# Kernel tuning notes

Hardware: AMD Instinct MI355X
Metric: run time of the kernel (lower is better)

## Reference

```python
import jax, jax.numpy as jnp
import numpy as np

NUM_USERS = 100000
NUM_ITEMS = 100000
N_NODES = NUM_USERS + NUM_ITEMS
EMB = 64
N_EDGES = 3200000
N_LAYERS = 3


def setup_inputs() -> dict:
    key = jax.random.key(0)
    k1, k2, k3, k4, k5 = jax.random.split(key, 5)
    user_emb = jax.random.normal(k1, (NUM_USERS, EMB), dtype=jnp.float32)
    item_emb = jax.random.normal(k2, (NUM_ITEMS, EMB), dtype=jnp.float32)
    # COO representation of the normalized adjacency norm_adj (values ~ 1/sqrt(d_i d_j))
    edge_row = jax.random.randint(k3, (N_EDGES,), 0, N_NODES, dtype=jnp.int32)
    edge_col = jax.random.randint(k4, (N_EDGES,), 0, N_NODES, dtype=jnp.int32)
    edge_w = jax.random.uniform(k5, (N_EDGES,), dtype=jnp.float32)
    return {"user_emb": user_emb, "item_emb": item_emb, "edge_w": edge_w,
            "edge_row": edge_row, "edge_col": edge_col}


def _spmm(edge_row, edge_col, edge_w, x):
    # y[r] = sum_{e: row[e]==r} w[e] * x[col[e]]  ==  torch.sparse.mm(norm_adj, x)
    msgs = edge_w[:, None] * x[edge_col]  # [n_edges, E]
    return jax.ops.segment_sum(msgs, edge_row, num_segments=N_NODES)


def reference(user_emb, item_emb, edge_w, edge_row, edge_col):
    ego = jnp.concatenate([user_emb, item_emb], axis=0)  # [N, E]
    acc = jnp.zeros_like(ego)
    for _ in range(N_LAYERS):
        ego = _spmm(edge_row, edge_col, edge_w, ego)
        acc = acc + ego
    final = acc / N_LAYERS  # mean over the n_layers propagated embeddings
    user_all = final[:NUM_USERS]
    item_all = final[NUM_USERS:]
    return (user_all, item_all)
```

## Files before the change

kernel.cpp:

```cpp
#include <hip/hip_runtime.h>
#include <hip/hip_bf16.h>


constexpr int NUM_USERS = 100000;
constexpr int NUM_ITEMS = 100000;
constexpr int N_NODES   = NUM_USERS + NUM_ITEMS;
constexpr int EMB       = 64;
constexpr int N_EDGES   = 3200000;

constexpr int BUCK_SHIFT = 8;
constexpr int NBUCK = (N_NODES + 255) >> BUCK_SHIFT;
constexpr int BIN_BLOCK = 512;
constexpr int EPB = 8192;
constexpr int NBIN_BLOCKS = (N_EDGES + EPB - 1) / EPB;
constexpr int SORT_CAP = 6144;

constexpr int HIST_BLOCKS   = 512;
constexpr int CONCAT_BLOCKS = (N_NODES * 8 + 255) / 256;

constexpr int ROWS_PER_BLOCK = 32;
constexpr int ECAP = 1536;


__device__ __forceinline__ float bfl(unsigned u) { return __uint_as_float(u << 16); }
__device__ __forceinline__ float bfh(unsigned u) { return __uint_as_float(u & 0xFFFF0000u); }
__device__ __forceinline__ unsigned f2bf(float f) {
    unsigned u = __float_as_uint(f);
    return (u + 0x7FFFu + ((u >> 16) & 1u)) >> 16;
}
__device__ __forceinline__ unsigned pk(float lo, float hi) {
    return f2bf(lo) | (f2bf(hi) << 16);
}


__global__ __launch_bounds__(256) void prep(
    const int* __restrict__ row, int* __restrict__ bcnt,
    const float4* __restrict__ u, const float4* __restrict__ it,
    uint4* __restrict__ ebuf) {
    __shared__ int h[NBUCK];
    if (blockIdx.x < HIST_BLOCKS) {
        for (int i = threadIdx.x; i < NBUCK; i += 256) h[i] = 0;
        __syncthreads();
        int nt = HIST_BLOCKS * 256;
        for (int e = blockIdx.x * 256 + threadIdx.x; e < N_EDGES; e += nt) {
            int r = __builtin_nontemporal_load(&row[e]);
            atomicAdd(&h[r >> BUCK_SHIFT], 1);
        }
        __syncthreads();
        for (int i = threadIdx.x; i < NBUCK; i += 256) {
            int c = h[i];
            if (c) atomicAdd(&bcnt[i], c);
        }
    } else {
        int i = (blockIdx.x - HIST_BLOCKS) * 256 + threadIdx.x;
        if (i >= N_NODES * 8) return;
        const float4* s = (i < NUM_USERS * 8) ? (u + 2 * (size_t)i)
                                              : (it + 2 * ((size_t)i - (size_t)NUM_USERS * 8));
        float4 f0 = s[0], f1 = s[1];
        uint4 o;
        o.x = pk(f0.x, f0.y); o.y = pk(f0.z, f0.w);
        o.z = pk(f1.x, f1.y); o.w = pk(f1.z, f1.w);
        ebuf[i] = o;
    }
}


__global__ __launch_bounds__(1024) void scan_buckets(const int* __restrict__ bcnt,
                                                     int* __restrict__ bbase,
                                                     int* __restrict__ bcursor) {
    __shared__ int lds[1024];
    int t = threadIdx.x;
    int v = (t < NBUCK) ? bcnt[t] : 0;
    lds[t] = v;
    __syncthreads();
    for (int off = 1; off < 1024; off <<= 1) {
        int x = (t >= off) ? lds[t - off] : 0;
        __syncthreads();
        lds[t] += x;
        __syncthreads();
    }
    int excl = lds[t] - v;
    if (t < NBUCK) { bbase[t] = excl; bcursor[t] = excl; }
    if (t == 0) bbase[NBUCK] = N_EDGES;
}

__global__ __launch_bounds__(BIN_BLOCK) void bin_edges(
    const int* __restrict__ row, const int* __restrict__ col,
    const float* __restrict__ w,
    int* __restrict__ bcursor,
    unsigned* __restrict__ binned_cw, unsigned char* __restrict__ binned_rl) {
    __shared__ unsigned      stage_cw[EPB];
    __shared__ unsigned char stage_rl[EPB];
    __shared__ int  hcnt[NBUCK];
    __shared__ int  hbase[NBUCK];
    __shared__ int  cursor[NBUCK];
    __shared__ int  lds2[BIN_BLOCK];
    int t = threadIdx.x;
    int e0 = blockIdx.x * EPB;
    int e1 = e0 + EPB; if (e1 > N_EDGES) e1 = N_EDGES;

    for (int i = t; i < NBUCK; i += BIN_BLOCK) hcnt[i] = 0;
    __syncthreads();
    for (int e = e0 + t; e < e1; e += BIN_BLOCK)
        atomicAdd(&hcnt[row[e] >> BUCK_SHIFT], 1);
    __syncthreads();

    for (int i = t; i < NBUCK; i += BIN_BLOCK) {
        int c = hcnt[i];
        hbase[i] = c ? atomicAdd(&bcursor[i], c) : 0;
    }
    int i0 = 2 * t, i1 = 2 * t + 1;
    int c0 = (i0 < NBUCK) ? hcnt[i0] : 0;
    int c1 = (i1 < NBUCK) ? hcnt[i1] : 0;
    lds2[t] = c0 + c1;
    __syncthreads();
    for (int off = 1; off < BIN_BLOCK; off <<= 1) {
        int x = (t >= off) ? lds2[t - off] : 0;
        __syncthreads();
        lds2[t] += x;
        __syncthreads();
    }
    int pairExcl = lds2[t] - (c0 + c1);
    if (i0 < NBUCK) cursor[i0] = pairExcl;
    if (i1 < NBUCK) cursor[i1] = pairExcl + c0;
    __syncthreads();

    for (int e = e0 + t; e < e1; e += BIN_BLOCK) {
        int r  = row[e];
        int bk = r >> BUCK_SHIFT;
        int pos = atomicAdd(&cursor[bk], 1);
        float wv = __builtin_nontemporal_load(&w[e]);
        unsigned q = (unsigned)(wv * 16384.f + 0.5f);
        if (q > 16383u) q = 16383u;
        stage_cw[pos] = (unsigned)__builtin_nontemporal_load(&col[e]) | (q << 18);
        stage_rl[pos] = (unsigned char)(r & 255);
    }
    __syncthreads();

    int wave = t >> 6;
    int lane = t & 63;
    int sl   = lane & 7;
    constexpr int NWAVE = BIN_BLOCK / 64;
    for (int base = wave * 8; base < NBUCK; base += NWAVE * 8) {
        int bk = base + (lane >> 3);
        if (bk < NBUCK) {
            int c  = hcnt[bk];
            int st = cursor[bk] - c;
            int gp = hbase[bk];
            for (int j = sl; j < c; j += 8) {
                binned_cw[gp + j] = stage_cw[st + j];
                binned_rl[gp + j] = stage_rl[st + j];
            }
        }
    }
}

__global__ __launch_bounds__(256) void sort_bucket(
    const int* __restrict__ bbase,
    const unsigned* __restrict__ binned_cw, const unsigned char* __restrict__ binned_rl,
    unsigned* __restrict__ sorted, int* __restrict__ row_start) {
    __shared__ unsigned      raw_cw[SORT_CAP];
    __shared__ unsigned char raw_rl[SORT_CAP];
    __shared__ unsigned      buf[SORT_CAP];
    __shared__ int cnt[256];
    __shared__ int sc[256];
    int b = blockIdx.x, t = threadIdx.x;
    int gb = bbase[b];
    int n  = bbase[b + 1] - gb;
    int m  = n < SORT_CAP ? n : SORT_CAP;

    cnt[t] = 0;
    for (int i = t; i < m; i += 256) {
        raw_cw[i] = binned_cw[gb + i];
        raw_rl[i] = binned_rl[gb + i];
    }
    __syncthreads();
    for (int i = t; i < m; i += 256)
        atomicAdd(&cnt[raw_rl[i]], 1);
    __syncthreads();

    int v = cnt[t];
    sc[t] = v;
    __syncthreads();
    for (int off = 1; off < 256; off <<= 1) {
        int x = (t >= off) ? sc[t - off] : 0;
        __syncthreads();
        sc[t] += x;
        __syncthreads();
    }
    int excl = sc[t] - v;

    int r = (b << BUCK_SHIFT) + t;
    if (r < N_NODES) row_start[r] = gb + excl;
    if (b == NBUCK - 1 && t == 0) row_start[N_NODES] = N_EDGES;
    __syncthreads();
    cnt[t] = excl;
    __syncthreads();

    for (int i = t; i < m; i += 256) {
        int k = atomicAdd(&cnt[raw_rl[i]], 1);
        buf[k] = raw_cw[i];
    }
    __syncthreads();
    for (int i = t; i < m; i += 256)
        sorted[gb + i] = buf[i];
}


template<bool LAST>
__global__ __launch_bounds__(256) void spmm_bf16(
    const int* __restrict__ row_start, const unsigned* __restrict__ sorted,
    const uint4* __restrict__ src,
    uint4* __restrict__ y,
    const uint4* __restrict__ y1,
    float4* __restrict__ out)
{
    __shared__ unsigned erec[ECAP];
    __shared__ int rs[ROWS_PER_BLOCK + 1];
    int t  = threadIdx.x;
    int R0 = blockIdx.x * ROWS_PER_BLOCK;
    if (t <= ROWS_PER_BLOCK) rs[t] = row_start[R0 + t];
    __syncthreads();
    int eb0 = rs[0];
    int n   = rs[ROWS_PER_BLOCK] - eb0;

    int g = t >> 3;
    int s = t & 7;
    int r = R0 + g;
    int s0 = rs[g], s1 = rs[g + 1];
    int cnt = s1 - s0;

    float a0 = 0.f, a1 = 0.f, a2 = 0.f, a3 = 0.f;
    float a4 = 0.f, a5 = 0.f, a6 = 0.f, a7 = 0.f;
    constexpr float WSC = 1.0f / 16384.f;

#define ACC(vv, wt) \
    a0 = fmaf(wt, bfl(vv.x), a0); a1 = fmaf(wt, bfh(vv.x), a1); \
    a2 = fmaf(wt, bfl(vv.y), a2); a3 = fmaf(wt, bfh(vv.y), a3); \
    a4 = fmaf(wt, bfl(vv.z), a4); a5 = fmaf(wt, bfh(vv.z), a5); \
    a6 = fmaf(wt, bfl(vv.w), a6); a7 = fmaf(wt, bfh(vv.w), a7);

    if (n <= ECAP) {
        for (int i = t; i < n; i += 256) erec[i] = sorted[eb0 + i];
        __syncthreads();
        int lb = s0 - eb0;
        for (int k = 0; k < cnt; k += 8) {
            int   c[8]; float wv[8]; uint4 gr[8];
#pragma unroll
            for (int j = 0; j < 8; ++j) {
                int lk = k + j;
                bool v = lk < cnt;
                unsigned e = erec[lb + (v ? lk : 0)];
                c[j]  = v ? (int)(e & 0x3FFFFu) : 0;
                wv[j] = v ? (float)(e >> 18) * WSC : 0.f;
            }
#pragma unroll
            for (int j = 0; j < 8; ++j) gr[j] = src[(size_t)c[j] * 8 + s];
#pragma unroll
            for (int j = 0; j < 8; ++j) { ACC(gr[j], wv[j]) }
        }
    } else {
        for (int k = 0; k < cnt; k += 8) {
            int   c[8]; float wv[8]; uint4 gr[8];
#pragma unroll
            for (int j = 0; j < 8; ++j) {
                int lk = k + j;
                bool v = lk < cnt;
                unsigned e = sorted[s0 + (v ? lk : 0)];
                c[j]  = v ? (int)(e & 0x3FFFFu) : 0;
                wv[j] = v ? (float)(e >> 18) * WSC : 0.f;
            }
#pragma unroll
            for (int j = 0; j < 8; ++j) gr[j] = src[(size_t)c[j] * 8 + s];
#pragma unroll
            for (int j = 0; j < 8; ++j) { ACC(gr[j], wv[j]) }
        }
    }
#undef ACC

    if (!LAST) {
        uint4 o;
        o.x = pk(a0, a1); o.y = pk(a2, a3);
        o.z = pk(a4, a5); o.w = pk(a6, a7);
        y[(size_t)r * 8 + s] = o;
    } else {
        uint4 u1 = y1[(size_t)r * 8 + s];
        uint4 u2 = src[(size_t)r * 8 + s];
        constexpr float sc = 1.0f / 3.0f;
        float4 o0, o1;
        o0.x = (a0 + bfl(u1.x) + bfl(u2.x)) * sc;
        o0.y = (a1 + bfh(u1.x) + bfh(u2.x)) * sc;
        o0.z = (a2 + bfl(u1.y) + bfl(u2.y)) * sc;
        o0.w = (a3 + bfh(u1.y) + bfh(u2.y)) * sc;
        o1.x = (a4 + bfl(u1.z) + bfl(u2.z)) * sc;
        o1.y = (a5 + bfh(u1.z) + bfh(u2.z)) * sc;
        o1.z = (a6 + bfl(u1.w) + bfl(u2.w)) * sc;
        o1.w = (a7 + bfh(u1.w) + bfh(u2.w)) * sc;
        size_t ob = (size_t)r * 16 + 2 * s;
        out[ob]     = o0;
        out[ob + 1] = o1;
    }
}


extern "C" void kernel_launch(void* const* d_in, const int* in_sizes, int n_in,
                              void* d_out, int out_size, void* d_ws, size_t ws_size,
                              hipStream_t stream) {
    const float* user_emb = (const float*)d_in[0];
    const float* item_emb = (const float*)d_in[1];
    const float* edge_w   = (const float*)d_in[2];
    const int*   edge_row = (const int*)d_in[3];
    const int*   edge_col = (const int*)d_in[4];

    char* p = (char*)d_ws;
    uint4*    ebuf = (uint4*)p;      p += (size_t)N_NODES * 8 * sizeof(uint4);
    uint4*    ybuf = (uint4*)p;      p += (size_t)N_NODES * 8 * sizeof(uint4);
    unsigned* sorted = (unsigned*)p; p += (size_t)N_EDGES * sizeof(unsigned);
    int*   bcnt = (int*)p;           p += (size_t)NBUCK * sizeof(int);
    int*   bbase = (int*)p;          p += (size_t)(NBUCK + 1) * sizeof(int);
    int*   bcursor = (int*)p;        p += (size_t)NBUCK * sizeof(int);
    int*   row_start = (int*)p;      p += (size_t)(N_NODES + 1) * sizeof(int);
    unsigned*      binned_cw = (unsigned*)ybuf;
    unsigned char* binned_rl = (unsigned char*)(ybuf) + (size_t)N_EDGES * 4;

    hipMemsetAsync(bcnt, 0, (size_t)NBUCK * sizeof(int), stream);

    prep<<<HIST_BLOCKS + CONCAT_BLOCKS, 256, 0, stream>>>(
        edge_row, bcnt, (const float4*)user_emb, (const float4*)item_emb, ebuf);

    scan_buckets<<<1, 1024, 0, stream>>>(bcnt, bbase, bcursor);
    bin_edges<<<NBIN_BLOCKS, BIN_BLOCK, 0, stream>>>(edge_row, edge_col, edge_w,
                                                     bcursor, binned_cw, binned_rl);
    sort_bucket<<<NBUCK, 256, 0, stream>>>(bbase, binned_cw, binned_rl,
                                           sorted, row_start);

    int grid = N_NODES / ROWS_PER_BLOCK;
    spmm_bf16<false><<<grid, 256, 0, stream>>>(row_start, sorted, ebuf, ybuf,
                                               nullptr, nullptr);
    spmm_bf16<false><<<grid, 256, 0, stream>>>(row_start, sorted, ybuf, ebuf,
                                               nullptr, nullptr);
    spmm_bf16<true><<<grid, 256, 0, stream>>>(row_start, sorted, ebuf, nullptr,
                                              ybuf, (float4*)d_out);
}
```

Before: 392.9 us.

## Fuse per-bucket row sort into each SpMM layer, dropping the global sort pass

Removes the separate sort_bucket kernel and the global sorted/row_start arrays. Each SpMM layer now loads its 256-row bucket of binned edges into shared memory, counting-sorts them by local row in place, then gathers and accumulates with 1024-thread blocks covering 256 rows. This saves one kernel launch and the sorted-array write and read, but repeats the bucket sort three times, once per layer. It also switches to fewer, larger blocks (782 blocks of 1024 threads) that use about 56KB of shared memory each, which may lower occupancy.

```diff
diff --git a/kernel.cpp b/kernel.cpp
--- a/kernel.cpp
+++ b/kernel.cpp
@@ -13,13 +13,10 @@
 constexpr int BIN_BLOCK = 512;
 constexpr int EPB = 8192;
 constexpr int NBIN_BLOCKS = (N_EDGES + EPB - 1) / EPB;
-constexpr int SORT_CAP = 6144;
+constexpr int FCAP = 6144;
 
 constexpr int HIST_BLOCKS   = 512;
 constexpr int CONCAT_BLOCKS = (N_NODES * 8 + 255) / 256;
-
-constexpr int ROWS_PER_BLOCK = 32;
-constexpr int ECAP = 1536;
 
 
 __device__ __forceinline__ float bfl(unsigned u) { return __uint_as_float(u << 16); }
@@ -155,83 +152,55 @@
     }
 }
 
-__global__ __launch_bounds__(256) void sort_bucket(
+
+template<bool LAST>
+__global__ __launch_bounds__(1024) void spmm_fused(
     const int* __restrict__ bbase,
     const unsigned* __restrict__ binned_cw, const unsigned char* __restrict__ binned_rl,
-    unsigned* __restrict__ sorted, int* __restrict__ row_start) {
-    __shared__ unsigned      raw_cw[SORT_CAP];
-    __shared__ unsigned char raw_rl[SORT_CAP];
-    __shared__ unsigned      buf[SORT_CAP];
-    __shared__ int cnt[256];
-    __shared__ int sc[256];
-    int b = blockIdx.x, t = threadIdx.x;
-    int gb = bbase[b];
-    int n  = bbase[b + 1] - gb;
-    int m  = n < SORT_CAP ? n : SORT_CAP;
-
-    cnt[t] = 0;
-    for (int i = t; i < m; i += 256) {
-        raw_cw[i] = binned_cw[gb + i];
-        raw_rl[i] = binned_rl[gb + i];
-    }
-    __syncthreads();
-    for (int i = t; i < m; i += 256)
-        atomicAdd(&cnt[raw_rl[i]], 1);
-    __syncthreads();
-
-    int v = cnt[t];
-    sc[t] = v;
-    __syncthreads();
-    for (int off = 1; off < 256; off <<= 1) {
-        int x = (t >= off) ? sc[t - off] : 0;
-        __syncthreads();
-        sc[t] += x;
-        __syncthreads();
-    }
-    int excl = sc[t] - v;
-
-    int r = (b << BUCK_SHIFT) + t;
-    if (r < N_NODES) row_start[r] = gb + excl;
-    if (b == NBUCK - 1 && t == 0) row_start[N_NODES] = N_EDGES;
-    __syncthreads();
-    cnt[t] = excl;
-    __syncthreads();
-
-    for (int i = t; i < m; i += 256) {
-        int k = atomicAdd(&cnt[raw_rl[i]], 1);
-        buf[k] = raw_cw[i];
-    }
-    __syncthreads();
-    for (int i = t; i < m; i += 256)
-        sorted[gb + i] = buf[i];
-}
-
-
-template<bool LAST>
-__global__ __launch_bounds__(256) void spmm_bf16(
-    const int* __restrict__ row_start, const unsigned* __restrict__ sorted,
     const uint4* __restrict__ src,
     uint4* __restrict__ y,
     const uint4* __restrict__ y1,
     float4* __restrict__ out)
 {
-    __shared__ unsigned erec[ECAP];
-    __shared__ int rs[ROWS_PER_BLOCK + 1];
-    int t  = threadIdx.x;
-    int R0 = blockIdx.x * ROWS_PER_BLOCK;
-    if (t <= ROWS_PER_BLOCK) rs[t] = row_start[R0 + t];
-    __syncthreads();
-    int eb0 = rs[0];
-    int n   = rs[ROWS_PER_BLOCK] - eb0;
+    __shared__ unsigned      raw_cw[FCAP];
+    __shared__ unsigned char raw_rl[FCAP];
+    __shared__ unsigned      buf[FCAP];
+    __shared__ int cnt[256], sc[256], cur[256];
+    int b = blockIdx.x, t = threadIdx.x;
+    int gb = bbase[b];
+    int n  = bbase[b + 1] - gb;
+    int m  = n < FCAP ? n : FCAP;
+
+    if (t < 256) cnt[t] = 0;
+    for (int i = t; i < m; i += 1024) {
+        raw_cw[i] = binned_cw[gb + i];
+        raw_rl[i] = binned_rl[gb + i];
+    }
+    __syncthreads();
+    for (int i = t; i < m; i += 1024)
+        atomicAdd(&cnt[raw_rl[i]], 1);
+    __syncthreads();
+
+    int v = 0;
+    if (t < 256) { v = cnt[t]; sc[t] = v; }
+    __syncthreads();
+    for (int off = 1; off < 256; off <<= 1) {
+        int x = (t >= off && t < 256) ? sc[t - off] : 0;
+        __syncthreads();
+        if (t < 256) sc[t] += x;
+        __syncthreads();
+    }
+    if (t < 256) cur[t] = sc[t] - v;
+    __syncthreads();
+
+    for (int i = t; i < m; i += 1024) {
+        int k = atomicAdd(&cur[raw_rl[i]], 1);
+        buf[k] = raw_cw[i];
+    }
+    __syncthreads();
 
     int g = t >> 3;
     int s = t & 7;
-    int r = R0 + g;
-    int s0 = rs[g], s1 = rs[g + 1];
-    int cnt = s1 - s0;
-
-    float a0 = 0.f, a1 = 0.f, a2 = 0.f, a3 = 0.f;
-    float a4 = 0.f, a5 = 0.f, a6 = 0.f, a7 = 0.f;
     constexpr float WSC = 1.0f / 16384.f;
 
 #define ACC(vv, wt) \
@@ -240,66 +209,55 @@
     a4 = fmaf(wt, bfl(vv.z), a4); a5 = fmaf(wt, bfh(vv.z), a5); \
     a6 = fmaf(wt, bfl(vv.w), a6); a7 = fmaf(wt, bfh(vv.w), a7);
 
-    if (n <= ECAP) {
-        for (int i = t; i < n; i += 256) erec[i] = sorted[eb0 + i];
-        __syncthreads();
-        int lb = s0 - eb0;
-        for (int k = 0; k < cnt; k += 8) {
+    for (int rr = g; rr < 256; rr += 128) {
+        int r = (b << 8) + rr;
+        if (r >= N_NODES) break;
+        int ct = cnt[rr];
+        int st = sc[rr] - ct;
+
+        float a0 = 0.f, a1 = 0.f, a2 = 0.f, a3 = 0.f;
+        float a4 = 0.f, a5 = 0.f, a6 = 0.f, a7 = 0.f;
+
+        for (int k = 0; k < ct; k += 8) {
             int   c[8]; float wv[8]; uint4 gr[8];
 #pragma unroll
             for (int j = 0; j < 8; ++j) {
                 int lk = k + j;
-                bool v = lk < cnt;
-                unsigned e = erec[lb + (v ? lk : 0)];
-                c[j]  = v ? (int)(e & 0x3FFFFu) : 0;
-                wv[j] = v ? (float)(e >> 18) * WSC : 0.f;
+                bool vv = lk < ct;
+                unsigned e = buf[st + (vv ? lk : 0)];
+                c[j]  = vv ? (int)(e & 0x3FFFFu) : 0;
+                wv[j] = vv ? (float)(e >> 18) * WSC : 0.f;
             }
 #pragma unroll
             for (int j = 0; j < 8; ++j) gr[j] = src[(size_t)c[j] * 8 + s];
 #pragma unroll
             for (int j = 0; j < 8; ++j) { ACC(gr[j], wv[j]) }
         }
-    } else {
-        for (int k = 0; k < cnt; k += 8) {
-            int   c[8]; float wv[8]; uint4 gr[8];
-#pragma unroll
-            for (int j = 0; j < 8; ++j) {
-                int lk = k + j;
-                bool v = lk < cnt;
-                unsigned e = sorted[s0 + (v ? lk : 0)];
-                c[j]  = v ? (int)(e & 0x3FFFFu) : 0;
-                wv[j] = v ? (float)(e >> 18) * WSC : 0.f;
-            }
-#pragma unroll
-            for (int j = 0; j < 8; ++j) gr[j] = src[(size_t)c[j] * 8 + s];
-#pragma unroll
-            for (int j = 0; j < 8; ++j) { ACC(gr[j], wv[j]) }
+
+        if (!LAST) {
+            uint4 o;
+            o.x = pk(a0, a1); o.y = pk(a2, a3);
+            o.z = pk(a4, a5); o.w = pk(a6, a7);
+            y[(size_t)r * 8 + s] = o;
+        } else {
+            uint4 u1 = y1[(size_t)r * 8 + s];
+            uint4 u2 = src[(size_t)r * 8 + s];
+            constexpr float scv = 1.0f / 3.0f;
+            float4 o0, o1;
+            o0.x = (a0 + bfl(u1.x) + bfl(u2.x)) * scv;
+            o0.y = (a1 + bfh(u1.x) + bfh(u2.x)) * scv;
+            o0.z = (a2 + bfl(u1.y) + bfl(u2.y)) * scv;
+            o0.w = (a3 + bfh(u1.y) + bfh(u2.y)) * scv;
+            o1.x = (a4 + bfl(u1.z) + bfl(u2.z)) * scv;
+            o1.y = (a5 + bfh(u1.z) + bfh(u2.z)) * scv;
+            o1.z = (a6 + bfl(u1.w) + bfl(u2.w)) * scv;
+            o1.w = (a7 + bfh(u1.w) + bfh(u2.w)) * scv;
+            size_t ob = (size_t)r * 16 + 2 * s;
+            out[ob]     = o0;
+            out[ob + 1] = o1;
         }
     }
 #undef ACC
-
-    if (!LAST) {
-        uint4 o;
-        o.x = pk(a0, a1); o.y = pk(a2, a3);
-        o.z = pk(a4, a5); o.w = pk(a6, a7);
-        y[(size_t)r * 8 + s] = o;
-    } else {
-        uint4 u1 = y1[(size_t)r * 8 + s];
-        uint4 u2 = src[(size_t)r * 8 + s];
-        constexpr float sc = 1.0f / 3.0f;
-        float4 o0, o1;
-        o0.x = (a0 + bfl(u1.x) + bfl(u2.x)) * sc;
-        o0.y = (a1 + bfh(u1.x) + bfh(u2.x)) * sc;
-        o0.z = (a2 + bfl(u1.y) + bfl(u2.y)) * sc;
-        o0.w = (a3 + bfh(u1.y) + bfh(u2.y)) * sc;
-        o1.x = (a4 + bfl(u1.z) + bfl(u2.z)) * sc;
-        o1.y = (a5 + bfh(u1.z) + bfh(u2.z)) * sc;
-        o1.z = (a6 + bfl(u1.w) + bfl(u2.w)) * sc;
-        o1.w = (a7 + bfh(u1.w) + bfh(u2.w)) * sc;
-        size_t ob = (size_t)r * 16 + 2 * s;
-        out[ob]     = o0;
-        out[ob + 1] = o1;
-    }
 }
 
 
@@ -315,13 +273,11 @@
     char* p = (char*)d_ws;
     uint4*    ebuf = (uint4*)p;      p += (size_t)N_NODES * 8 * sizeof(uint4);
     uint4*    ybuf = (uint4*)p;      p += (size_t)N_NODES * 8 * sizeof(uint4);
-    unsigned* sorted = (unsigned*)p; p += (size_t)N_EDGES * sizeof(unsigned);
+    unsigned* binned_cw = (unsigned*)p;      p += (size_t)N_EDGES * sizeof(unsigned);
+    unsigned char* binned_rl = (unsigned char*)p; p += (size_t)N_EDGES;
     int*   bcnt = (int*)p;           p += (size_t)NBUCK * sizeof(int);
     int*   bbase = (int*)p;          p += (size_t)(NBUCK + 1) * sizeof(int);
     int*   bcursor = (int*)p;        p += (size_t)NBUCK * sizeof(int);
-    int*   row_start = (int*)p;      p += (size_t)(N_NODES + 1) * sizeof(int);
-    unsigned*      binned_cw = (unsigned*)ybuf;
-    unsigned char* binned_rl = (unsigned char*)(ybuf) + (size_t)N_EDGES * 4;
 
     hipMemsetAsync(bcnt, 0, (size_t)NBUCK * sizeof(int), stream);
 
@@ -331,14 +287,11 @@
     scan_buckets<<<1, 1024, 0, stream>>>(bcnt, bbase, bcursor);
     bin_edges<<<NBIN_BLOCKS, BIN_BLOCK, 0, stream>>>(edge_row, edge_col, edge_w,
                                                      bcursor, binned_cw, binned_rl);
-    sort_bucket<<<NBUCK, 256, 0, stream>>>(bbase, binned_cw, binned_rl,
-                                           sorted, row_start);
-
-    int grid = N_NODES / ROWS_PER_BLOCK;
-    spmm_bf16<false><<<grid, 256, 0, stream>>>(row_start, sorted, ebuf, ybuf,
-                                               nullptr, nullptr);
-    spmm_bf16<false><<<grid, 256, 0, stream>>>(row_start, sorted, ybuf, ebuf,
-                                               nullptr, nullptr);
-    spmm_bf16<true><<<grid, 256, 0, stream>>>(row_start, sorted, ebuf, nullptr,
-                                              ybuf, (float4*)d_out);
-}
+
+    spmm_fused<false><<<NBUCK, 1024, 0, stream>>>(bbase, binned_cw, binned_rl,
+                                                  ebuf, ybuf, nullptr, nullptr);
+    spmm_fused<false><<<NBUCK, 1024, 0, stream>>>(bbase, binned_cw, binned_rl,
+                                                  ybuf, ebuf, nullptr, nullptr);
+    spmm_fused<true><<<NBUCK, 1024, 0, stream>>>(bbase, binned_cw, binned_rl,
+                                                 ebuf, nullptr, ybuf, (float4*)d_out);
+}
```

New measurement: 409.3 us. 1.04x slower.
